# Kernel optimization log

Hardware: AMD Instinct MI355X
Metric: run time of the kernel (lower is better)

Reference implementation:

```python
import jax, jax.numpy as jnp
import numpy as np

H = 128  # hidden_size

def _lstm_layer(x, w_ih, w_hh, b_ih, b_hh):
    # x: [B, T, D]; w_ih: [4H, D]; w_hh: [4H, H]; biases: [4H]
    B, T, _ = x.shape
    # Precompute input contributions for all timesteps (the big GEMM).
    xg = jnp.einsum('btd,gd->btg', x, w_ih) + b_ih + b_hh  # [B, T, 4H]
    xg = jnp.transpose(xg, (1, 0, 2))  # [T, B, 4H]
    w_hh_t = w_hh.T  # [H, 4H]

    def step(carry, xt):
        h, c = carry
        g = xt + h @ w_hh_t  # [B, 4H]
        i, f, gg, o = jnp.split(g, 4, axis=-1)  # PyTorch gate order i,f,g,o
        i = jax.nn.sigmoid(i)
        f = jax.nn.sigmoid(f)
        gg = jnp.tanh(gg)
        o = jax.nn.sigmoid(o)
        c = f * c + i * gg
        h = o * jnp.tanh(c)
        return (h, c), h

    h0 = jnp.zeros((B, H), dtype=x.dtype)
    c0 = jnp.zeros((B, H), dtype=x.dtype)
    _, hs = jax.lax.scan(step, (h0, c0), xg)  # hs: [T, B, H]
    return jnp.transpose(hs, (1, 0, 2))  # [B, T, H]

def setup_inputs() -> dict:
    key = jax.random.key(0)
    ks = jax.random.split(key, 11)
    s = 1.0 / np.sqrt(H)  # PyTorch LSTM init scale
    return {
        'x': jax.random.normal(ks[0], (128, 512, 1024), dtype=jnp.float32),
        'w_ih0': jax.random.normal(ks[1], (4 * H, 1024), dtype=jnp.float32) * s,
        'w_hh0': jax.random.normal(ks[2], (4 * H, H), dtype=jnp.float32) * s,
        'b_ih0': jax.random.normal(ks[3], (4 * H,), dtype=jnp.float32) * s,
        'b_hh0': jax.random.normal(ks[4], (4 * H,), dtype=jnp.float32) * s,
        'w_ih1': jax.random.normal(ks[5], (4 * H, H), dtype=jnp.float32) * s,
        'w_hh1': jax.random.normal(ks[6], (4 * H, H), dtype=jnp.float32) * s,
        'b_ih1': jax.random.normal(ks[7], (4 * H,), dtype=jnp.float32) * s,
        'b_hh1': jax.random.normal(ks[8], (4 * H,), dtype=jnp.float32) * s,
        'fc_w': jax.random.normal(ks[9], (8, H), dtype=jnp.float32) * s,
        'fc_b': jax.random.normal(ks[10], (8,), dtype=jnp.float32) * s,
    }

def reference(x, w_ih0, w_hh0, b_ih0, b_hh0, w_ih1, w_hh1, b_ih1, b_hh1, fc_w, fc_b):
    h1 = _lstm_layer(x, w_ih0, w_hh0, b_ih0, b_hh0)   # [B, T, H]
    h2 = _lstm_layer(h1, w_ih1, w_hh1, b_ih1, b_hh1)  # [B, T, H]
    logits = h2[:, -1, :] @ fc_w.T + fc_b             # [B, num_classes]
    return logits
```

## Files before the change

### kernel.cpp

```cpp
#include <hip/hip_runtime.h>
#include <hip/hip_bf16.h>

#define BATCH 128
#define TSTEPS 512
#define HID 128
#define GATES 512
#define M_TOTAL (BATCH * TSTEPS)

typedef _Float16 h2_t  __attribute__((ext_vector_type(2)));
typedef _Float16 half4 __attribute__((ext_vector_type(4)));
typedef _Float16 half8 __attribute__((ext_vector_type(8)));
typedef float    f32x4 __attribute__((ext_vector_type(4)));

__device__ __forceinline__ float sigmoidf_fast(float x) {
    return 1.0f / (1.0f + __expf(-x));
}
__device__ __forceinline__ float tanhf_fast(float x) {
    return 1.0f - 2.0f / (__expf(2.0f * x) + 1.0f);
}
__device__ __forceinline__ float fdot2h(h2_t a, h2_t b, float c) {
#if __has_builtin(__builtin_amdgcn_fdot2)
    return __builtin_amdgcn_fdot2(a, b, c, false);
#else
    return c + (float)a[0] * (float)b[0] + (float)a[1] * (float)b[1];
#endif
}

__global__ __launch_bounds__(256) void convert_w(
    const float* __restrict__ src, _Float16* __restrict__ hi, _Float16* __restrict__ lo)
{
    const int i = blockIdx.x * 256 + threadIdx.x;
    float4 v = ((const float4*)src)[i];
    half4 h, l;
    h[0] = (_Float16)v.x; l[0] = (_Float16)(v.x - (float)h[0]);
    h[1] = (_Float16)v.y; l[1] = (_Float16)(v.y - (float)h[1]);
    h[2] = (_Float16)v.z; l[2] = (_Float16)(v.z - (float)h[2]);
    h[3] = (_Float16)v.w; l[3] = (_Float16)(v.w - (float)h[3]);
    *(half4*)&hi[4 * i] = h;
    *(half4*)&lo[4 * i] = l;
}

__global__ __launch_bounds__(256, 2) void gemm_mfma(
    const float* __restrict__ A,
    const _Float16* __restrict__ Wh,
    const _Float16* __restrict__ Wl,
    const float* __restrict__ b0,
    const float* __restrict__ b1,
    float* __restrict__ xg)
{
    constexpr int K = 1024;
    __shared__ __align__(16) _Float16 sXh[128 * 32];
    __shared__ __align__(16) _Float16 sXl[128 * 32];
    __shared__ __align__(16) _Float16 sWh[128 * 32];
    __shared__ __align__(16) _Float16 sWl[128 * 32];

    const int tid = threadIdx.x;
    const int lane = tid & 63, wv = tid >> 6;
    const int wm = wv & 1, wn = wv >> 1;
    const int n0 = blockIdx.x * 128;
    const int m0 = blockIdx.y * 128;

    const int ar = tid & 127, aks = (tid >> 7) * 16;
    const float* pA = A + (size_t)(m0 + ar) * K + aks;
    const _Float16* pWh0 = Wh + (size_t)(n0 + (tid & 127)) * K + (tid >> 7) * 8;
    const _Float16* pWl0 = Wl + (size_t)(n0 + (tid & 127)) * K + (tid >> 7) * 8;

    f32x4 acc[4][4];
    #pragma unroll
    for (int nt = 0; nt < 4; ++nt) {
        const int cn = n0 + wn * 64 + nt * 16 + (lane & 15);
        const float bv = b0[cn] + b1[cn];
        #pragma unroll
        for (int mt = 0; mt < 4; ++mt) acc[mt][nt] = (f32x4){bv, bv, bv, bv};
    }

    float xv[16];
    half8 w0h, w1h, w0l, w1l;
    #pragma unroll
    for (int j = 0; j < 4; ++j) *(float4*)&xv[4 * j] = *(const float4*)(pA + 4 * j);
    w0h = *(const half8*)(pWh0);      w1h = *(const half8*)(pWh0 + 16);
    w0l = *(const half8*)(pWl0);      w1l = *(const half8*)(pWl0 + 16);

    const int kb0 = (tid >> 7) * 2;
    for (int ks = 0; ks < 32; ++ks) {
        half8 hh0, hh1, hl0, hl1;
        #pragma unroll
        for (int j = 0; j < 8; ++j) {
            _Float16 h = (_Float16)xv[j];
            hh0[j] = h; hl0[j] = (_Float16)(xv[j] - (float)h);
        }
        #pragma unroll
        for (int j = 0; j < 8; ++j) {
            _Float16 h = (_Float16)xv[8 + j];
            hh1[j] = h; hl1[j] = (_Float16)(xv[8 + j] - (float)h);
        }
        if (ks) __syncthreads();
        *(half8*)&sXh[(size_t)((kb0    ) * 128 + ar) * 8] = hh0;
        *(half8*)&sXh[(size_t)((kb0 + 1) * 128 + ar) * 8] = hh1;
        *(half8*)&sXl[(size_t)((kb0    ) * 128 + ar) * 8] = hl0;
        *(half8*)&sXl[(size_t)((kb0 + 1) * 128 + ar) * 8] = hl1;
        *(half8*)&sWh[(size_t)tid * 8]         = w0h;
        *(half8*)&sWh[(size_t)(tid + 256) * 8] = w1h;
        *(half8*)&sWl[(size_t)tid * 8]         = w0l;
        *(half8*)&sWl[(size_t)(tid + 256) * 8] = w1l;
        __syncthreads();

        if (ks < 31) {
            const int kn = (ks + 1) * 32;
            #pragma unroll
            for (int j = 0; j < 4; ++j)
                *(float4*)&xv[4 * j] = *(const float4*)(pA + kn + 4 * j);
            w0h = *(const half8*)(pWh0 + kn);      w1h = *(const half8*)(pWh0 + kn + 16);
            w0l = *(const half8*)(pWl0 + kn);      w1l = *(const half8*)(pWl0 + kn + 16);
        }

        const int fr = lane & 15, kb = lane >> 4;
        half8 ah[4], al[4], bh[4], bl[4];
        #pragma unroll
        for (int mt = 0; mt < 4; ++mt) {
            const int idx = (kb * 128 + wm * 64 + mt * 16 + fr) * 8;
            ah[mt] = *(const half8*)&sXh[idx];
            al[mt] = *(const half8*)&sXl[idx];
        }
        #pragma unroll
        for (int nt = 0; nt < 4; ++nt) {
            const int idx = (kb * 128 + wn * 64 + nt * 16 + fr) * 8;
            bh[nt] = *(const half8*)&sWh[idx];
            bl[nt] = *(const half8*)&sWl[idx];
        }
        #pragma unroll
        for (int mt = 0; mt < 4; ++mt)
            #pragma unroll
            for (int nt = 0; nt < 4; ++nt) {
                acc[mt][nt] = __builtin_amdgcn_mfma_f32_16x16x32_f16(ah[mt], bh[nt], acc[mt][nt], 0, 0, 0);
                acc[mt][nt] = __builtin_amdgcn_mfma_f32_16x16x32_f16(ah[mt], bl[nt], acc[mt][nt], 0, 0, 0);
                acc[mt][nt] = __builtin_amdgcn_mfma_f32_16x16x32_f16(al[mt], bh[nt], acc[mt][nt], 0, 0, 0);
            }
    }

    #pragma unroll
    for (int mt = 0; mt < 4; ++mt) {
        const int rm = m0 + wm * 64 + mt * 16 + (lane >> 4) * 4;
        #pragma unroll
        for (int nt = 0; nt < 4; ++nt) {
            const int cn = n0 + wn * 64 + nt * 16 + (lane & 15);
            #pragma unroll
            for (int r = 0; r < 4; ++r)
                xg[(size_t)(rm + r) * GATES + cn] = acc[mt][nt][r];
        }
    }
}

__global__ __launch_bounds__(512, 2) void fused_rec2(
    const float* __restrict__ xg,
    const float* __restrict__ w_hh0,
    const float* __restrict__ w_ih1,
    const float* __restrict__ w_hh1,
    const float* __restrict__ b_ih1,
    const float* __restrict__ b_hh1,
    const float* __restrict__ fc_w,
    const float* __restrict__ fc_b,
    unsigned int* __restrict__ h1g,
    int* __restrict__ flags,
    float* __restrict__ logits)
{
    const int blk = blockIdx.x;
    const bool L1 = blk >= BATCH;
    const int b = blk & (BATCH - 1);
    const int g = threadIdx.x;

    __shared__ __align__(16) _Float16 h16[HID];
    __shared__ __align__(16) float act_s[GATES];
    __shared__ __align__(16) unsigned int hin[8][64];
    __shared__ __align__(16) float hfin[HID];

    h2_t whh[64], wih[64];
    {
        const float4* w4 = (const float4*)((L1 ? w_hh1 : w_hh0) + (size_t)g * HID);
        #pragma unroll
        for (int i = 0; i < 32; ++i) {
            float4 v = w4[i];
            whh[2 * i]     = (h2_t){(_Float16)v.x, (_Float16)v.y};
            whh[2 * i + 1] = (h2_t){(_Float16)v.z, (_Float16)v.w};
        }
    }
    float bias = 0.f;
    if (L1) {
        const float4* w4 = (const float4*)(w_ih1 + (size_t)g * HID);
        #pragma unroll
        for (int i = 0; i < 32; ++i) {
            float4 v = w4[i];
            wih[2 * i]     = (h2_t){(_Float16)v.x, (_Float16)v.y};
            wih[2 * i + 1] = (h2_t){(_Float16)v.z, (_Float16)v.w};
        }
        bias = b_ih1[g] + b_hh1[g];
    }

    if (g < HID) h16[g] = (_Float16)0.f;
    float c = 0.f;

    unsigned int* h1row = h1g + (size_t)b * TSTEPS * 64;
    int* flagb = flags + b * 64;

    if (L1 && g < 64) {
        while (__hip_atomic_load(&flagb[g], __ATOMIC_ACQUIRE, __HIP_MEMORY_SCOPE_AGENT) < 8) {}
        #pragma unroll
        for (int d = 0; d < 8; ++d)
            hin[d][g] = __hip_atomic_load(&h1row[(size_t)d * 64 + g],
                                          __ATOMIC_RELAXED, __HIP_MEMORY_SCOPE_AGENT);
    }

    const float* xgb = xg + (size_t)b * TSTEPS * GATES + g;
    float xcur[4], xnxt[4];
    if (!L1) {
        #pragma unroll
        for (int u = 0; u < 4; ++u) xcur[u] = xgb[(size_t)u * GATES];
    }
    __syncthreads();

    for (int t4 = 0; t4 < 128; ++t4) {
        if (!L1) {
            const int tn = (t4 + 1 < 128) ? (t4 + 1) * 4 : t4 * 4;
            #pragma unroll
            for (int u = 0; u < 4; ++u) xnxt[u] = xgb[(size_t)(tn + u) * GATES];
        }
        #pragma unroll
        for (int u = 0; u < 4; ++u) {
            const int t = t4 * 4 + u;
            float p0 = 0.f, p1 = 0.f, p2 = 0.f, p3 = 0.f;
            {
                const half8* hv = (const half8*)h16;
                #pragma unroll
                for (int j = 0; j < 16; ++j) {
                    half8 hh = hv[j];
                    p0 = fdot2h(whh[4 * j],     (h2_t){hh[0], hh[1]}, p0);
                    p1 = fdot2h(whh[4 * j + 1], (h2_t){hh[2], hh[3]}, p1);
                    p2 = fdot2h(whh[4 * j + 2], (h2_t){hh[4], hh[5]}, p2);
                    p3 = fdot2h(whh[4 * j + 3], (h2_t){hh[6], hh[7]}, p3);
                }
            }
            if (L1) {
                const half8* xv8 = (const half8*)&hin[t & 7][0];
                #pragma unroll
                for (int j = 0; j < 16; ++j) {
                    half8 hh = xv8[j];
                    p0 = fdot2h(wih[4 * j],     (h2_t){hh[0], hh[1]}, p0);
                    p1 = fdot2h(wih[4 * j + 1], (h2_t){hh[2], hh[3]}, p1);
                    p2 = fdot2h(wih[4 * j + 2], (h2_t){hh[4], hh[5]}, p2);
                    p3 = fdot2h(wih[4 * j + 3], (h2_t){hh[6], hh[7]}, p3);
                }
            }
            const float s = (p0 + p1) + (p2 + p3) + (L1 ? bias : xcur[u]);
            act_s[g] = ((g >> 7) == 2) ? tanhf_fast(s) : sigmoidf_fast(s);
            __syncthreads();
            if (g < HID) {
                const float ig = act_s[g];
                const float fg = act_s[g + 128];
                const float gg = act_s[g + 256];
                const float og = act_s[g + 384];
                c = __fmaf_rn(fg, c, ig * gg);
                const float h = og * tanhf_fast(c);
                h16[g] = (_Float16)h;
                if (L1 && t == TSTEPS - 1) hfin[g] = h;
            }
            __syncthreads();
            if (!L1 && g < 64) {
                __hip_atomic_store(&h1row[(size_t)t * 64 + g], ((const unsigned int*)h16)[g],
                                   __ATOMIC_RELAXED, __HIP_MEMORY_SCOPE_AGENT);
                if (u == 3)
                    __hip_atomic_store(&flagb[g], t + 1,
                                       __ATOMIC_RELEASE, __HIP_MEMORY_SCOPE_AGENT);
            }
            if (L1 && g < 64 && u == 3) {
                const int tgt = t + 5;
                if (tgt + 3 < TSTEPS) {
                    while (__hip_atomic_load(&flagb[g], __ATOMIC_ACQUIRE,
                                             __HIP_MEMORY_SCOPE_AGENT) < tgt + 4) {}
                    #pragma unroll
                    for (int d = 0; d < 4; ++d)
                        hin[(tgt + d) & 7][g] =
                            __hip_atomic_load(&h1row[(size_t)(tgt + d) * 64 + g],
                                              __ATOMIC_RELAXED, __HIP_MEMORY_SCOPE_AGENT);
                }
            }
        }
        if (!L1) {
            xcur[0] = xnxt[0]; xcur[1] = xnxt[1]; xcur[2] = xnxt[2]; xcur[3] = xnxt[3];
        }
    }

    if (L1) {
        __syncthreads();
        if (g < 8) {
            float s2 = fc_b[g];
            const float* wr = fc_w + g * HID;
            #pragma unroll 4
            for (int k2 = 0; k2 < HID; ++k2) s2 = __fmaf_rn(wr[k2], hfin[k2], s2);
            logits[b * 8 + g] = s2;
        }
    }
}

extern "C" void kernel_launch(void* const* d_in, const int* in_sizes, int n_in,
                              void* d_out, int out_size, void* d_ws, size_t ws_size,
                              hipStream_t stream) {
    const float* x     = (const float*)d_in[0];
    const float* w_ih0 = (const float*)d_in[1];
    const float* w_hh0 = (const float*)d_in[2];
    const float* b_ih0 = (const float*)d_in[3];
    const float* b_hh0 = (const float*)d_in[4];
    const float* w_ih1 = (const float*)d_in[5];
    const float* w_hh1 = (const float*)d_in[6];
    const float* b_ih1 = (const float*)d_in[7];
    const float* b_hh1 = (const float*)d_in[8];
    const float* fc_w  = (const float*)d_in[9];
    const float* fc_b  = (const float*)d_in[10];
    float* out = (float*)d_out;

    char* ws = (char*)d_ws;
    float*        xgb   = (float*)ws;
    _Float16*     Whp   = (_Float16*)(ws + (size_t)M_TOTAL * GATES * 4);
    _Float16*     Wlp   = (_Float16*)(ws + (size_t)M_TOTAL * GATES * 4 + 1048576);
    unsigned int* h1g   = (unsigned int*)(ws + (size_t)M_TOTAL * GATES * 4 + 2097152);
    int*          flags = (int*)(ws + (size_t)M_TOTAL * GATES * 4 + 2097152
                                    + (size_t)BATCH * TSTEPS * 64 * 4);

    convert_w<<<dim3(512), dim3(256), 0, stream>>>(w_ih0, Whp, Wlp);
    gemm_mfma<<<dim3(4, 512), dim3(256), 0, stream>>>(x, Whp, Wlp, b_ih0, b_hh0, xgb);
    fused_rec2<<<dim3(2 * BATCH), dim3(512), 0, stream>>>(
        xgb, w_hh0, w_ih1, w_hh1, b_ih1, b_hh1, fc_w, fc_b, h1g, flags, out);
}
```

Before: 1.496 ms.

## Split recurrent matvec over K across threads with shared-memory gate reduction

Each thread now computes partial dot products for four gates (i, f, g, o of one hidden unit) over a 32-wide slice of the hidden vector, instead of one full 128-length gate row. It reads 4 instead of 16 half8 vectors from LDS per step. The partials are written to a padded shared buffer, and the first 128 threads sum them and apply all four activations themselves. This cuts per-thread LDS traffic and the dependent dot-product chain on the serial recurrence path. In exchange, the 128 reducing threads do more serial transcendental work, and there is an extra 16-float shared read per step.

```diff
diff --git a/kernel.cpp b/kernel.cpp
--- a/kernel.cpp
+++ b/kernel.cpp
@@ -167,50 +167,59 @@
     const int blk = blockIdx.x;
     const bool L1 = blk >= BATCH;
     const int b = blk & (BATCH - 1);
-    const int g = threadIdx.x;
+    const int tid = threadIdx.x;
+    const int ks = tid >> 7;
+    const int gq = tid & 127;
 
     __shared__ __align__(16) _Float16 h16[HID];
-    __shared__ __align__(16) float act_s[GATES];
+    __shared__ __align__(16) float part[128 * 20];
     __shared__ __align__(16) unsigned int hin[8][64];
     __shared__ __align__(16) float hfin[HID];
 
-    h2_t whh[64], wih[64];
+    h2_t wh[4][16], wi[4][16];
     {
-        const float4* w4 = (const float4*)((L1 ? w_hh1 : w_hh0) + (size_t)g * HID);
-        #pragma unroll
-        for (int i = 0; i < 32; ++i) {
-            float4 v = w4[i];
-            whh[2 * i]     = (h2_t){(_Float16)v.x, (_Float16)v.y};
-            whh[2 * i + 1] = (h2_t){(_Float16)v.z, (_Float16)v.w};
+        const float* wsrc = (L1 ? w_hh1 : w_hh0);
+        #pragma unroll
+        for (int q = 0; q < 4; ++q) {
+            const float4* w4 = (const float4*)(wsrc + (size_t)(gq + 128 * q) * HID + 32 * ks);
+            #pragma unroll
+            for (int i = 0; i < 8; ++i) {
+                float4 v = w4[i];
+                wh[q][2 * i]     = (h2_t){(_Float16)v.x, (_Float16)v.y};
+                wh[q][2 * i + 1] = (h2_t){(_Float16)v.z, (_Float16)v.w};
+            }
         }
     }
     float bias = 0.f;
     if (L1) {
-        const float4* w4 = (const float4*)(w_ih1 + (size_t)g * HID);
-        #pragma unroll
-        for (int i = 0; i < 32; ++i) {
-            float4 v = w4[i];
-            wih[2 * i]     = (h2_t){(_Float16)v.x, (_Float16)v.y};
-            wih[2 * i + 1] = (h2_t){(_Float16)v.z, (_Float16)v.w};
-        }
-        bias = b_ih1[g] + b_hh1[g];
-    }
-
-    if (g < HID) h16[g] = (_Float16)0.f;
+        #pragma unroll
+        for (int q = 0; q < 4; ++q) {
+            const float4* w4 = (const float4*)(w_ih1 + (size_t)(gq + 128 * q) * HID + 32 * ks);
+            #pragma unroll
+            for (int i = 0; i < 8; ++i) {
+                float4 v = w4[i];
+                wi[q][2 * i]     = (h2_t){(_Float16)v.x, (_Float16)v.y};
+                wi[q][2 * i + 1] = (h2_t){(_Float16)v.z, (_Float16)v.w};
+            }
+        }
+        bias = b_ih1[tid] + b_hh1[tid];
+    }
+
+    if (tid < HID) h16[tid] = (_Float16)0.f;
     float c = 0.f;
 
     unsigned int* h1row = h1g + (size_t)b * TSTEPS * 64;
     int* flagb = flags + b * 64;
 
-    if (L1 && g < 64) {
-        while (__hip_atomic_load(&flagb[g], __ATOMIC_ACQUIRE, __HIP_MEMORY_SCOPE_AGENT) < 8) {}
+    if (L1 && tid < 64) {
+        while (__hip_atomic_load(&flagb[tid], __ATOMIC_ACQUIRE, __HIP_MEMORY_SCOPE_AGENT) < 8) {}
         #pragma unroll
         for (int d = 0; d < 8; ++d)
-            hin[d][g] = __hip_atomic_load(&h1row[(size_t)d * 64 + g],
-                                          __ATOMIC_RELAXED, __HIP_MEMORY_SCOPE_AGENT);
-    }
-
-    const float* xgb = xg + (size_t)b * TSTEPS * GATES + g;
+            hin[d][tid] = __hip_atomic_load(&h1row[(size_t)d * 64 + tid],
+                                            __ATOMIC_RELAXED, __HIP_MEMORY_SCOPE_AGENT);
+    }
+
+    const float* xgb = xg + (size_t)b * TSTEPS * GATES + tid;
     float xcur[4], xnxt[4];
     if (!L1) {
         #pragma unroll
@@ -229,57 +238,79 @@
             const int t = t4 * 4 + u;
             float p0 = 0.f, p1 = 0.f, p2 = 0.f, p3 = 0.f;
             {
-                const half8* hv = (const half8*)h16;
+                const half8* hv8 = ((const half8*)h16) + 4 * ks;
                 #pragma unroll
-                for (int j = 0; j < 16; ++j) {
-                    half8 hh = hv[j];
-                    p0 = fdot2h(whh[4 * j],     (h2_t){hh[0], hh[1]}, p0);
-                    p1 = fdot2h(whh[4 * j + 1], (h2_t){hh[2], hh[3]}, p1);
-                    p2 = fdot2h(whh[4 * j + 2], (h2_t){hh[4], hh[5]}, p2);
-                    p3 = fdot2h(whh[4 * j + 3], (h2_t){hh[6], hh[7]}, p3);
+                for (int jj = 0; jj < 4; ++jj) {
+                    half8 hh = hv8[jj];
+                    #pragma unroll
+                    for (int e = 0; e < 4; ++e) {
+                        h2_t hp = (h2_t){hh[2 * e], hh[2 * e + 1]};
+                        p0 = fdot2h(wh[0][4 * jj + e], hp, p0);
+                        p1 = fdot2h(wh[1][4 * jj + e], hp, p1);
+                        p2 = fdot2h(wh[2][4 * jj + e], hp, p2);
+                        p3 = fdot2h(wh[3][4 * jj + e], hp, p3);
+                    }
                 }
             }
             if (L1) {
-                const half8* xv8 = (const half8*)&hin[t & 7][0];
+                float q0 = 0.f, q1 = 0.f, q2 = 0.f, q3 = 0.f;
+                const half8* xv8 = ((const half8*)&hin[t & 7][0]) + 4 * ks;
                 #pragma unroll
-                for (int j = 0; j < 16; ++j) {
-                    half8 hh = xv8[j];
-                    p0 = fdot2h(wih[4 * j],     (h2_t){hh[0], hh[1]}, p0);
-                    p1 = fdot2h(wih[4 * j + 1], (h2_t){hh[2], hh[3]}, p1);
-                    p2 = fdot2h(wih[4 * j + 2], (h2_t){hh[4], hh[5]}, p2);
-                    p3 = fdot2h(wih[4 * j + 3], (h2_t){hh[6], hh[7]}, p3);
+                for (int jj = 0; jj < 4; ++jj) {
+                    half8 hh = xv8[jj];
+                    #pragma unroll
+                    for (int e = 0; e < 4; ++e) {
+                        h2_t hp = (h2_t){hh[2 * e], hh[2 * e + 1]};
+                        q0 = fdot2h(wi[0][4 * jj + e], hp, q0);
+                        q1 = fdot2h(wi[1][4 * jj + e], hp, q1);
+                        q2 = fdot2h(wi[2][4 * jj + e], hp, q2);
+                        q3 = fdot2h(wi[3][4 * jj + e], hp, q3);
+                    }
                 }
-            }
-            const float s = (p0 + p1) + (p2 + p3) + (L1 ? bias : xcur[u]);
-            act_s[g] = ((g >> 7) == 2) ? tanhf_fast(s) : sigmoidf_fast(s);
+                p0 += q0; p1 += q1; p2 += q2; p3 += q3;
+            }
+            {
+                const float extra = L1 ? bias : xcur[u];
+                if      (ks == 0) p0 += extra;
+                else if (ks == 1) p1 += extra;
+                else if (ks == 2) p2 += extra;
+                else              p3 += extra;
+            }
+            *(f32x4*)&part[gq * 20 + ks * 4] = (f32x4){p0, p1, p2, p3};
             __syncthreads();
-            if (g < HID) {
-                const float ig = act_s[g];
-                const float fg = act_s[g + 128];
-                const float gg = act_s[g + 256];
-                const float og = act_s[g + 384];
+            if (tid < HID) {
+                const f32x4* pr = (const f32x4*)&part[tid * 20];
+                f32x4 v0 = pr[0], v1 = pr[1], v2 = pr[2], v3 = pr[3];
+                const float si = (v0[0] + v1[0]) + (v2[0] + v3[0]);
+                const float sf = (v0[1] + v1[1]) + (v2[1] + v3[1]);
+                const float sg = (v0[2] + v1[2]) + (v2[2] + v3[2]);
+                const float so = (v0[3] + v1[3]) + (v2[3] + v3[3]);
+                const float ig = sigmoidf_fast(si);
+                const float fg = sigmoidf_fast(sf);
+                const float gg = tanhf_fast(sg);
+                const float og = sigmoidf_fast(so);
                 c = __fmaf_rn(fg, c, ig * gg);
                 const float h = og * tanhf_fast(c);
-                h16[g] = (_Float16)h;
-                if (L1 && t == TSTEPS - 1) hfin[g] = h;
+                h16[tid] = (_Float16)h;
+                if (L1 && t == TSTEPS - 1) hfin[tid] = h;
             }
             __syncthreads();
-            if (!L1 && g < 64) {
-                __hip_atomic_store(&h1row[(size_t)t * 64 + g], ((const unsigned int*)h16)[g],
+            if (!L1 && tid < 64) {
+                __hip_atomic_store(&h1row[(size_t)t * 64 + tid], ((const unsigned int*)h16)[tid],
                                    __ATOMIC_RELAXED, __HIP_MEMORY_SCOPE_AGENT);
                 if (u == 3)
-                    __hip_atomic_store(&flagb[g], t + 1,
+                    __hip_atomic_store(&flagb[tid], t + 1,
                                        __ATOMIC_RELEASE, __HIP_MEMORY_SCOPE_AGENT);
             }
-            if (L1 && g < 64 && u == 3) {
+            if (L1 && tid < 64 && u == 3) {
                 const int tgt = t + 5;
                 if (tgt + 3 < TSTEPS) {
-                    while (__hip_atomic_load(&flagb[g], __ATOMIC_ACQUIRE,
+                    while (__hip_atomic_load(&flagb[tid], __ATOMIC_ACQUIRE,
                                              __HIP_MEMORY_SCOPE_AGENT) < tgt + 4) {}
                     #pragma unroll
                     for (int d = 0; d < 4; ++d)
-                        hin[(tgt + d) & 7][g] =
-                            __hip_atomic_load(&h1row[(size_t)(tgt + d) * 64 + g],
+                        hin[(tgt + d) & 7][tid] =
+                            __hip_atomic_load(&h1row[(size_t)(tgt + d) * 64 + tid],
                                               __ATOMIC_RELAXED, __HIP_MEMORY_SCOPE_AGENT);
                 }
             }
@@ -291,12 +322,12 @@
 
     if (L1) {
         __syncthreads();
-        if (g < 8) {
-            float s2 = fc_b[g];
-            const float* wr = fc_w + g * HID;
+        if (tid < 8) {
+            float s2 = fc_b[tid];
+            const float* wr = fc_w + tid * HID;
             #pragma unroll 4
             for (int k2 = 0; k2 < HID; ++k2) s2 = __fmaf_rn(wr[k2], hfin[k2], s2);
-            logits[b * 8 + g] = s2;
+            logits[b * 8 + tid] = s2;
         }
     }
 }
```

After: 1.494 ms. About the same (-0.1%).
